# Optimization experiments

Measured on AMD Instinct MI355X. Metric: run time of the kernel, lower is better.

The kernel has to match this reference:

```python
import jax, jax.numpy as jnp
import numpy as np

N_POINTS = 2_000_000
GRID = 256  # voxel grid resolution (D=H=W), production-scale stand-in for source's 128


def setup_inputs() -> dict:
    key = jax.random.key(0)
    k1, k2, k3 = jax.random.split(key, 3)
    coords = jax.random.uniform(k1, (N_POINTS, 3), dtype=jnp.float32,
                                minval=-0.95, maxval=0.95)
    registration_pred = jax.random.normal(k2, (N_POINTS, 3), dtype=jnp.float32) * 0.02
    registration_gt = jax.random.normal(k3, (N_POINTS, 3), dtype=jnp.float32) * 0.02
    return {"registration_pred": registration_pred,
            "registration_gt": registration_gt,
            "coords": coords}


def _splat(pts, size):
    """Trilinear scatter (adjoint of F.grid_sample, align_corners=False,
    zero padding). pts: [N,3] normalized coords in (x,y,z) order mapping to
    (W,H,D). Splats weight 1 per point. Returns [D,H,W] volume."""
    D = H = W = size
    # grid_sample align_corners=False unnormalization: p = ((g+1)*size - 1)/2
    x = ((pts[:, 0] + 1.0) * W - 1.0) * 0.5
    y = ((pts[:, 1] + 1.0) * H - 1.0) * 0.5
    z = ((pts[:, 2] + 1.0) * D - 1.0) * 0.5
    x0f, y0f, z0f = jnp.floor(x), jnp.floor(y), jnp.floor(z)
    fx, fy, fz = x - x0f, y - y0f, z - z0f  # fractional offsets
    x0, y0, z0 = x0f.astype(jnp.int32), y0f.astype(jnp.int32), z0f.astype(jnp.int32)
    vol = jnp.zeros(D * H * W, dtype=pts.dtype)
    for dz in (0, 1):
        wz = fz if dz else (1.0 - fz)
        for dy in (0, 1):
            wy = fy if dy else (1.0 - fy)
            for dx in (0, 1):
                wx = fx if dx else (1.0 - fx)
                xi, yi, zi = x0 + dx, y0 + dy, z0 + dz
                valid = ((xi >= 0) & (xi < W) & (yi >= 0) & (yi < H)
                         & (zi >= 0) & (zi < D))
                w = jnp.where(valid, wx * wy * wz, 0.0)
                idx = jnp.where(valid, (zi * H + yi) * W + xi, 0)
                vol = vol.at[idx].add(w)
    return vol.reshape(D, H, W)


def reference(registration_pred, registration_gt, coords):
    pred_vol = _splat(coords + registration_pred, GRID)
    gt_vol = _splat(coords + registration_gt, GRID)
    # HuberLoss(reduction='sum', delta=1.0)
    d = pred_vol - gt_vol
    ad = jnp.abs(d)
    return jnp.sum(jnp.where(ad <= 1.0, 0.5 * d * d, ad - 0.5))
```

## Files before the change

### kernel.cpp

```cpp
#include <hip/hip_runtime.h>

#define GRID_RES 256
#define NCELLS 1024
#define NB 1024
#define BCAP 6144
#define SCAP 4864
#define NPT 2

#define W_SCALE 2097152.0f
#define INV_W (1.0f / 2097152.0f)
#define L_SCALE 512.0f
#define INV_L (1.0f / 512.0f)

template <typename F>
__device__ __forceinline__ void enum_event(float px, float py, float pz,
                                           unsigned sign, F&& emit) {
    float x = ((px + 1.0f) * (float)GRID_RES - 1.0f) * 0.5f;
    float y = ((py + 1.0f) * (float)GRID_RES - 1.0f) * 0.5f;
    float z = ((pz + 1.0f) * (float)GRID_RES - 1.0f) * 0.5f;
    float xf = floorf(x), yf = floorf(y), zf = floorf(z);
    int x0 = (int)xf, y0 = (int)yf, z0 = (int)zf;
    unsigned qx = (unsigned)((x - xf) * 65535.0f + 0.5f);
    unsigned qy = (unsigned)((y - yf) * 65535.0f + 0.5f);
    unsigned qz = (unsigned)((z - zf) * 16383.0f + 0.5f);
    unsigned w0 = qx | (qy << 16);
    unsigned w1q = qz | (sign << 31);

    int cxs[2], cys[2], czs[2];
    int nx = 0, ny = 0, nz = 0;
    {
        bool vA = (x0 >= 0) & (x0 <= 255);
        bool vB = (x0 >= -1) & (x0 <= 254);
        int cA = x0 >> 5, cB = (x0 + 1) >> 5;
        if (vA) cxs[nx++] = cA;
        if (vB && (!vA || cB != cA)) cxs[nx++] = cB;
    }
    {
        bool vA = (y0 >= 0) & (y0 <= 255);
        bool vB = (y0 >= -1) & (y0 <= 254);
        int cA = y0 >> 5, cB = (y0 + 1) >> 5;
        if (vA) cys[ny++] = cA;
        if (vB && (!vA || cB != cA)) cys[ny++] = cB;
    }
    {
        bool vA = (z0 >= 0) & (z0 <= 255);
        bool vB = (z0 >= -1) & (z0 <= 254);
        int cA = z0 >> 4, cB = (z0 + 1) >> 4;
        if (vA) czs[nz++] = cA;
        if (vB && (!vA || cB != cA)) czs[nz++] = cB;
    }
    for (int a = 0; a < nz; ++a) {
        int cz = czs[a];
        unsigned lz = (unsigned)(z0 - (cz << 4) + 1);
        for (int b = 0; b < ny; ++b) {
            int cy = cys[b];
            unsigned ly = (unsigned)(y0 - (cy << 5) + 1);
            for (int c = 0; c < nx; ++c) {
                int cx = cxs[c];
                unsigned lx = (unsigned)(x0 - (cx << 5) + 1);
                int cell = (cz << 6) | (cy << 3) | cx;
                unsigned w1 = w1q | (lx << 14) | (ly << 20) | (lz << 26);
                emit(cell, w0, w1);
            }
        }
    }
}

__global__ __launch_bounds__(1024) void bin_kernel(
    const float* __restrict__ pred, const float* __restrict__ gt,
    const float* __restrict__ coords, unsigned* __restrict__ pkT,
    uint2* __restrict__ payload, int* __restrict__ lossAcc, int n) {
    __shared__ unsigned short sC[SCAP];
    __shared__ unsigned sW0[SCAP];
    __shared__ unsigned sW1[SCAP];
    __shared__ unsigned h[NCELLS];
    __shared__ unsigned wtot[16];
    __shared__ unsigned scnt;
    int b = blockIdx.x;
    int t = threadIdx.x;
    if (b == 0 && t == 0) { lossAcc[0] = 0; lossAcc[1] = 0; }
    h[t] = 0;
    if (t == 0) scnt = 0;
    __syncthreads();

    int chunk = (n + NB - 1) / NB;
    int start = b * chunk;
    int end = min(start + chunk, n);
    const float3* c3 = (const float3*)coords;
    const float3* p3 = (const float3*)pred;
    const float3* g3 = (const float3*)gt;

    auto stage = [&](int cell, unsigned w0, unsigned w1) {
        unsigned slot = atomicAdd(&scnt, 1u);
        if (slot < (unsigned)SCAP) {
            sC[slot] = (unsigned short)cell;
            sW0[slot] = w0;
            sW1[slot] = w1;
            atomicAdd(&h[cell], 1u);
        }
    };
#pragma unroll
    for (int k = 0; k < NPT; ++k) {
        int i = start + t + (k << 10);
        if (i < end) {
            float3 c = c3[i];
            float3 p = p3[i];
            float3 g = g3[i];
            enum_event(c.x + p.x, c.y + p.y, c.z + p.z, 0u, stage);
            enum_event(c.x + g.x, c.y + g.y, c.z + g.z, 1u, stage);
        }
    }
    __syncthreads();

    unsigned x = h[t];
    unsigned incl = x;
    int lane = t & 63, wid = t >> 6;
#pragma unroll
    for (int off = 1; off < 64; off <<= 1) {
        unsigned y = __shfl_up(incl, off, 64);
        if (lane >= off) incl += y;
    }
    if (lane == 63) wtot[wid] = incl;
    __syncthreads();
    if (t == 0) {
        unsigned r = 0;
#pragma unroll
        for (int w = 0; w < 16; ++w) { unsigned v = wtot[w]; wtot[w] = r; r += v; }
    }
    __syncthreads();
    unsigned offE = incl - x + wtot[wid];
    pkT[(size_t)b * NCELLS + t] = offE | (x << 16);
    __syncthreads();
    h[t] = offE;
    __syncthreads();

    uint2* pb = payload + (size_t)b * BCAP;
    unsigned m = min(scnt, (unsigned)SCAP);
    for (unsigned j = t; j < m; j += 1024) {
        int cell = (int)sC[j];
        unsigned slot = atomicAdd(&h[cell], 1u);
        pb[slot] = make_uint2(sW0[j], sW1[j]);
    }
}

__global__ __launch_bounds__(1024) void accum_kernel(
    const uint2* __restrict__ payload, const unsigned* __restrict__ pkT,
    int* __restrict__ lossAcc, float* __restrict__ out) {
    __shared__ int v[16384];
    __shared__ unsigned sbase[NB + 1];
    __shared__ unsigned pbase[NB];
    __shared__ unsigned w16[16];
    __shared__ float wsum[16];
    int c = blockIdx.x;
    int t = threadIdx.x;
#pragma unroll
    for (int j = 0; j < 16; ++j) v[t + (j << 10)] = 0;

    int lane = t & 63, wid = t >> 6;
    unsigned pk = pkT[(size_t)t * NCELLS + c];
    unsigned off = pk & 0xFFFFu;
    unsigned cnt = pk >> 16;
    unsigned incl = cnt;
#pragma unroll
    for (int o = 1; o < 64; o <<= 1) {
        unsigned y = __shfl_up(incl, o, 64);
        if (lane >= o) incl += y;
    }
    if (lane == 63) w16[wid] = incl;
    __syncthreads();
    if (t == 0) {
        unsigned r = 0;
#pragma unroll
        for (int w = 0; w < 16; ++w) { unsigned q = w16[w]; w16[w] = r; r += q; }
    }
    __syncthreads();
    unsigned sb = incl - cnt + w16[wid];
    sbase[t] = sb;
    pbase[t] = (unsigned)t * (unsigned)BCAP + off;
    if (t == 1023) sbase[NB] = sb + cnt;
    __syncthreads();

    unsigned total = sbase[NB];
    for (unsigned i = t; i < total; i += 1024) {
        int lo = 0, hi = NB - 1;
#pragma unroll
        for (int s = 0; s < 10; ++s) {
            int mid = (lo + hi + 1) >> 1;
            if (sbase[mid] <= i) lo = mid; else hi = mid - 1;
        }
        uint2 p = payload[(size_t)pbase[lo] + (i - sbase[lo])];
        float fx = (float)(p.x & 0xFFFFu) * (1.0f / 65535.0f);
        float fy = (float)(p.x >> 16) * (1.0f / 65535.0f);
        float fz = (float)(p.y & 0x3FFFu) * (1.0f / 16383.0f);
        int lx = (int)((p.y >> 14) & 63u);
        int ly = (int)((p.y >> 20) & 63u);
        int lz = (int)((p.y >> 26) & 31u);
        float s = (p.y >> 31) ? -W_SCALE : W_SCALE;
        float wxs[2] = {1.0f - fx, fx};
        float wys[2] = {1.0f - fy, fy};
        float wzs[2] = {1.0f - fz, fz};
        int xb = lx - 1, yb = ly - 1, zb = lz - 1;
#pragma unroll
        for (int dz = 0; dz < 2; ++dz) {
            int rz = zb + dz;
            if ((unsigned)rz > 15u) continue;
            float wz = s * wzs[dz];
#pragma unroll
            for (int dy = 0; dy < 2; ++dy) {
                int ry = yb + dy;
                if ((unsigned)ry > 31u) continue;
                float wyz = wz * wys[dy];
#pragma unroll
                for (int dx = 0; dx < 2; ++dx) {
                    int rx = xb + dx;
                    if ((unsigned)rx > 31u) continue;
                    int iw = __float2int_rn(wyz * wxs[dx]);
                    atomicAdd(&v[(rz << 10) | (ry << 5) | rx], iw);
                }
            }
        }
    }
    __syncthreads();

    float acc = 0.0f;
#pragma unroll
    for (int j = 0; j < 16; ++j) {
        int val = v[t + (j << 10)];
        float d = (float)val * INV_W;
        float ad = fabsf(d);
        acc += (ad <= 1.0f) ? 0.5f * d * d : ad - 0.5f;
    }
#pragma unroll
    for (int o = 32; o > 0; o >>= 1) acc += __shfl_down(acc, o, 64);
    if (lane == 0) wsum[wid] = acc;
    __syncthreads();
    if (t == 0) {
        float tsum = 0.0f;
#pragma unroll
        for (int w = 0; w < 16; ++w) tsum += wsum[w];
        atomicAdd(&lossAcc[0], __float2int_rn(tsum * L_SCALE));
        __threadfence();
        unsigned old = atomicAdd((unsigned*)&lossAcc[1], 1u);
        if (old == (unsigned)(NCELLS - 1)) {
            __threadfence();
            int fin = atomicAdd(&lossAcc[0], 0);
            out[0] = (float)fin * INV_L;
        }
    }
}

extern "C" void kernel_launch(void* const* d_in, const int* in_sizes, int n_in,
                              void* d_out, int out_size, void* d_ws, size_t ws_size,
                              hipStream_t stream) {
    const float* reg_pred = (const float*)d_in[0];
    const float* reg_gt   = (const float*)d_in[1];
    const float* coords   = (const float*)d_in[2];
    float* out = (float*)d_out;

    char* ws = (char*)d_ws;
    int* lossAcc = (int*)ws;
    unsigned* pkT = (unsigned*)(ws + 256);
    uint2* payload = (uint2*)((char*)pkT + (size_t)NB * NCELLS * 4);

    int n = in_sizes[0] / 3;

    bin_kernel<<<NB, 1024, 0, stream>>>(reg_pred, reg_gt, coords, pkT,
                                        payload, lossAcc, n);
    accum_kernel<<<NCELLS, 1024, 0, stream>>>(payload, pkT, lossAcc, out);
}
```

Baseline: 183.3 us.

## Warp-aggregate staging slots, transpose bin table, accumulate two cells per block

In the binning kernel, each thread now counts its cell spans and a warp prefix scan reserves staging slots with one atomic per warp, replacing one shared atomic per emitted event. A separate transpose kernel makes the per-bin count table coalesced for the accumulation pass. Each accumulation block now handles two adjacent cells with a 128KB shared volume, which halves the block count and the per-block scan overhead. In exchange this adds a kernel launch, extra workspace, and heavier shared memory use per block, which lowers occupancy.

Measured after the change: 174.9 us. 4.6% less time.

```diff
diff --git a/kernel.cpp b/kernel.cpp
--- a/kernel.cpp
+++ b/kernel.cpp
@@ -3,18 +3,20 @@
 #define GRID_RES 256
 #define NCELLS 1024
 #define NB 1024
-#define BCAP 6144
-#define SCAP 4864
+#define SCAP 5120
+#define BCAP SCAP
 #define NPT 2
+#define APAIRS 512
 
 #define W_SCALE 2097152.0f
 #define INV_W (1.0f / 2097152.0f)
 #define L_SCALE 512.0f
 #define INV_L (1.0f / 512.0f)
 
-template <typename F>
-__device__ __forceinline__ void enum_event(float px, float py, float pz,
-                                           unsigned sign, F&& emit) {
+struct CEv { unsigned w0, w1q, xyz; };
+
+__device__ __forceinline__ CEv make_cev(float px, float py, float pz,
+                                        unsigned sign) {
     float x = ((px + 1.0f) * (float)GRID_RES - 1.0f) * 0.5f;
     float y = ((py + 1.0f) * (float)GRID_RES - 1.0f) * 0.5f;
     float z = ((pz + 1.0f) * (float)GRID_RES - 1.0f) * 0.5f;
@@ -23,9 +25,34 @@
     unsigned qx = (unsigned)((x - xf) * 65535.0f + 0.5f);
     unsigned qy = (unsigned)((y - yf) * 65535.0f + 0.5f);
     unsigned qz = (unsigned)((z - zf) * 16383.0f + 0.5f);
-    unsigned w0 = qx | (qy << 16);
-    unsigned w1q = qz | (sign << 31);
-
+    bool valid = (x0 >= -1) & (x0 <= 255) & (y0 >= -1) & (y0 <= 255) &
+                 (z0 >= -1) & (z0 <= 255);
+    CEv e;
+    e.w0 = qx | (qy << 16);
+    e.w1q = qz | (sign << 31);
+    e.xyz = valid ? ((unsigned)(x0 + 1) | ((unsigned)(y0 + 1) << 10) |
+                     ((unsigned)(z0 + 1) << 20) | (1u << 30))
+                  : 0u;
+    return e;
+}
+
+__device__ __forceinline__ int span_count(const CEv& e) {
+    if (!(e.xyz & (1u << 30))) return 0;
+    int x0 = (int)(e.xyz & 1023u) - 1;
+    int y0 = (int)((e.xyz >> 10) & 1023u) - 1;
+    int z0 = (int)((e.xyz >> 20) & 1023u) - 1;
+    int nx = (x0 >= 0) + ((x0 <= 254) & ((x0 < 0) | ((x0 & 31) == 31)));
+    int ny = (y0 >= 0) + ((y0 <= 254) & ((y0 < 0) | ((y0 & 31) == 31)));
+    int nz = (z0 >= 0) + ((z0 <= 254) & ((z0 < 0) | ((z0 & 15) == 15)));
+    return nx * ny * nz;
+}
+
+template <typename F>
+__device__ __forceinline__ void enum_cells(const CEv& e, F&& emit) {
+    if (!(e.xyz & (1u << 30))) return;
+    int x0 = (int)(e.xyz & 1023u) - 1;
+    int y0 = (int)((e.xyz >> 10) & 1023u) - 1;
+    int z0 = (int)((e.xyz >> 20) & 1023u) - 1;
     int cxs[2], cys[2], czs[2];
     int nx = 0, ny = 0, nz = 0;
     {
@@ -59,8 +86,8 @@
                 int cx = cxs[c];
                 unsigned lx = (unsigned)(x0 - (cx << 5) + 1);
                 int cell = (cz << 6) | (cy << 3) | cx;
-                unsigned w1 = w1q | (lx << 14) | (ly << 20) | (lz << 26);
-                emit(cell, w0, w1);
+                unsigned w1 = e.w1q | (lx << 14) | (ly << 20) | (lz << 26);
+                emit(cell, e.w0, w1);
             }
         }
     }
@@ -89,16 +116,9 @@
     const float3* c3 = (const float3*)coords;
     const float3* p3 = (const float3*)pred;
     const float3* g3 = (const float3*)gt;
-
-    auto stage = [&](int cell, unsigned w0, unsigned w1) {
-        unsigned slot = atomicAdd(&scnt, 1u);
-        if (slot < (unsigned)SCAP) {
-            sC[slot] = (unsigned short)cell;
-            sW0[slot] = w0;
-            sW1[slot] = w1;
-            atomicAdd(&h[cell], 1u);
-        }
-    };
+    int lane = t & 63, wid = t >> 6;
+
+    CEv ev[2 * NPT];
 #pragma unroll
     for (int k = 0; k < NPT; ++k) {
         int i = start + t + (k << 10);
@@ -106,21 +126,49 @@
             float3 c = c3[i];
             float3 p = p3[i];
             float3 g = g3[i];
-            enum_event(c.x + p.x, c.y + p.y, c.z + p.z, 0u, stage);
-            enum_event(c.x + g.x, c.y + g.y, c.z + g.z, 1u, stage);
-        }
-    }
+            ev[2 * k] = make_cev(c.x + p.x, c.y + p.y, c.z + p.z, 0u);
+            ev[2 * k + 1] = make_cev(c.x + g.x, c.y + g.y, c.z + g.z, 1u);
+        } else {
+            ev[2 * k].xyz = 0;
+            ev[2 * k + 1].xyz = 0;
+        }
+    }
+
+    unsigned mtot = 0;
+#pragma unroll
+    for (int k = 0; k < 2 * NPT; ++k) mtot += span_count(ev[k]);
+    unsigned incl = mtot;
+#pragma unroll
+    for (int o = 1; o < 64; o <<= 1) {
+        unsigned y = __shfl_up(incl, o, 64);
+        if (lane >= o) incl += y;
+    }
+    unsigned wbase = 0;
+    if (lane == 63) wbase = atomicAdd(&scnt, incl);
+    wbase = __shfl(wbase, 63, 64);
+    unsigned my = wbase + incl - mtot;
+
+#pragma unroll
+    for (int k = 0; k < 2 * NPT; ++k)
+        enum_cells(ev[k], [&](int cell, unsigned w0, unsigned w1) {
+            if (my < (unsigned)SCAP) {
+                sC[my] = (unsigned short)cell;
+                sW0[my] = w0;
+                sW1[my] = w1;
+                atomicAdd(&h[cell], 1u);
+            }
+            ++my;
+        });
     __syncthreads();
 
     unsigned x = h[t];
-    unsigned incl = x;
-    int lane = t & 63, wid = t >> 6;
-#pragma unroll
-    for (int off = 1; off < 64; off <<= 1) {
-        unsigned y = __shfl_up(incl, off, 64);
-        if (lane >= off) incl += y;
-    }
-    if (lane == 63) wtot[wid] = incl;
+    unsigned hincl = x;
+#pragma unroll
+    for (int o = 1; o < 64; o <<= 1) {
+        unsigned y = __shfl_up(hincl, o, 64);
+        if (lane >= o) hincl += y;
+    }
+    if (lane == 63) wtot[wid] = hincl;
     __syncthreads();
     if (t == 0) {
         unsigned r = 0;
@@ -128,7 +176,7 @@
         for (int w = 0; w < 16; ++w) { unsigned v = wtot[w]; wtot[w] = r; r += v; }
     }
     __syncthreads();
-    unsigned offE = incl - x + wtot[wid];
+    unsigned offE = hincl - x + wtot[wid];
     pkT[(size_t)b * NCELLS + t] = offE | (x << 16);
     __syncthreads();
     h[t] = offE;
@@ -143,23 +191,38 @@
     }
 }
 
+__global__ __launch_bounds__(256) void transpose_kernel(
+    const unsigned* __restrict__ src, unsigned* __restrict__ dst) {
+    __shared__ unsigned tile[64][65];
+    int bx = (blockIdx.x & 15) << 6;
+    int by = (blockIdx.x >> 4) << 6;
+    int tx = threadIdx.x & 63, ty = threadIdx.x >> 6;
+    for (int r = ty; r < 64; r += 4)
+        tile[r][tx] = src[(size_t)(by + r) * 1024 + bx + tx];
+    __syncthreads();
+    for (int r = ty; r < 64; r += 4)
+        dst[(size_t)(bx + r) * 1024 + by + tx] = tile[tx][r];
+}
+
 __global__ __launch_bounds__(1024) void accum_kernel(
-    const uint2* __restrict__ payload, const unsigned* __restrict__ pkT,
+    const uint2* __restrict__ payload, const unsigned* __restrict__ pkTT,
     int* __restrict__ lossAcc, float* __restrict__ out) {
-    __shared__ int v[16384];
+    __shared__ int v[32768];
     __shared__ unsigned sbase[NB + 1];
     __shared__ unsigned pbase[NB];
+    __shared__ unsigned short c0s[NB];
     __shared__ unsigned w16[16];
     __shared__ float wsum[16];
-    int c = blockIdx.x;
+    int p = blockIdx.x;
     int t = threadIdx.x;
 #pragma unroll
-    for (int j = 0; j < 16; ++j) v[t + (j << 10)] = 0;
+    for (int j = 0; j < 32; ++j) v[t + (j << 10)] = 0;
 
     int lane = t & 63, wid = t >> 6;
-    unsigned pk = pkT[(size_t)t * NCELLS + c];
-    unsigned off = pk & 0xFFFFu;
-    unsigned cnt = pk >> 16;
+    unsigned pk0 = pkTT[(size_t)(2 * p) * NB + t];
+    unsigned pk1 = pkTT[(size_t)(2 * p + 1) * NB + t];
+    unsigned cnt0 = pk0 >> 16;
+    unsigned cnt = cnt0 + (pk1 >> 16);
     unsigned incl = cnt;
 #pragma unroll
     for (int o = 1; o < 64; o <<= 1) {
@@ -176,7 +239,8 @@
     __syncthreads();
     unsigned sb = incl - cnt + w16[wid];
     sbase[t] = sb;
-    pbase[t] = (unsigned)t * (unsigned)BCAP + off;
+    pbase[t] = (unsigned)t * (unsigned)BCAP + (pk0 & 0xFFFFu);
+    c0s[t] = (unsigned short)cnt0;
     if (t == 1023) sbase[NB] = sb + cnt;
     __syncthreads();
 
@@ -188,14 +252,16 @@
             int mid = (lo + hi + 1) >> 1;
             if (sbase[mid] <= i) lo = mid; else hi = mid - 1;
         }
-        uint2 p = payload[(size_t)pbase[lo] + (i - sbase[lo])];
-        float fx = (float)(p.x & 0xFFFFu) * (1.0f / 65535.0f);
-        float fy = (float)(p.x >> 16) * (1.0f / 65535.0f);
-        float fz = (float)(p.y & 0x3FFFu) * (1.0f / 16383.0f);
-        int lx = (int)((p.y >> 14) & 63u);
-        int ly = (int)((p.y >> 20) & 63u);
-        int lz = (int)((p.y >> 26) & 31u);
-        float s = (p.y >> 31) ? -W_SCALE : W_SCALE;
+        unsigned j = i - sbase[lo];
+        unsigned half = (j < (unsigned)c0s[lo]) ? 0u : 16384u;
+        uint2 pp = payload[(size_t)pbase[lo] + j];
+        float fx = (float)(pp.x & 0xFFFFu) * (1.0f / 65535.0f);
+        float fy = (float)(pp.x >> 16) * (1.0f / 65535.0f);
+        float fz = (float)(pp.y & 0x3FFFu) * (1.0f / 16383.0f);
+        int lx = (int)((pp.y >> 14) & 63u);
+        int ly = (int)((pp.y >> 20) & 63u);
+        int lz = (int)((pp.y >> 26) & 31u);
+        float s = (pp.y >> 31) ? -W_SCALE : W_SCALE;
         float wxs[2] = {1.0f - fx, fx};
         float wys[2] = {1.0f - fy, fy};
         float wzs[2] = {1.0f - fz, fz};
@@ -215,7 +281,7 @@
                     int rx = xb + dx;
                     if ((unsigned)rx > 31u) continue;
                     int iw = __float2int_rn(wyz * wxs[dx]);
-                    atomicAdd(&v[(rz << 10) | (ry << 5) | rx], iw);
+                    atomicAdd(&v[half + (rz << 10) + (ry << 5) + rx], iw);
                 }
             }
         }
@@ -224,7 +290,7 @@
 
     float acc = 0.0f;
 #pragma unroll
-    for (int j = 0; j < 16; ++j) {
+    for (int j = 0; j < 32; ++j) {
         int val = v[t + (j << 10)];
         float d = (float)val * INV_W;
         float ad = fabsf(d);
@@ -241,7 +307,7 @@
         atomicAdd(&lossAcc[0], __float2int_rn(tsum * L_SCALE));
         __threadfence();
         unsigned old = atomicAdd((unsigned*)&lossAcc[1], 1u);
-        if (old == (unsigned)(NCELLS - 1)) {
+        if (old == (unsigned)(APAIRS - 1)) {
             __threadfence();
             int fin = atomicAdd(&lossAcc[0], 0);
             out[0] = (float)fin * INV_L;
@@ -259,12 +325,14 @@
 
     char* ws = (char*)d_ws;
     int* lossAcc = (int*)ws;
-    unsigned* pkT = (unsigned*)(ws + 256);
-    uint2* payload = (uint2*)((char*)pkT + (size_t)NB * NCELLS * 4);
+    unsigned* pkT  = (unsigned*)(ws + 256);
+    unsigned* pkTT = pkT + (size_t)NB * NCELLS;
+    uint2* payload = (uint2*)((char*)pkTT + (size_t)NB * NCELLS * 4);
 
     int n = in_sizes[0] / 3;
 
     bin_kernel<<<NB, 1024, 0, stream>>>(reg_pred, reg_gt, coords, pkT,
                                         payload, lossAcc, n);
-    accum_kernel<<<NCELLS, 1024, 0, stream>>>(payload, pkT, lossAcc, out);
-}
+    transpose_kernel<<<256, 256, 0, stream>>>(pkT, pkTT);
+    accum_kernel<<<APAIRS, 1024, 0, stream>>>(payload, pkTT, lossAcc, out);
+}
```
